# Performance work log

Measured on AMD Instinct MI355X. Metric: run time of the kernel, lower is better.

The kernel has to match this reference:

```python
import jax, jax.numpy as jnp
import numpy as np

INPUT_SIZE = 512
HIDDEN = 1024
OUT = 512
LN_EPS = 1e-5


def setup_inputs() -> dict:
    key = jax.random.key(0)
    ks = jax.random.split(key, 12)
    B, T = 128, 512
    def lin(k, fan_in, shape):
        bound = 1.0 / np.sqrt(fan_in)
        return jax.random.uniform(k, shape, jnp.float32, -bound, bound)
    in0 = INPUT_SIZE + HIDDEN
    in1 = HIDDEN + HIDDEN
    return {
        "x": jax.random.normal(ks[0], (B, T, INPUT_SIZE), jnp.float32),
        "W0": lin(ks[1], in0, (in0, 4 * HIDDEN)),
        "b0": lin(ks[2], in0, (4 * HIDDEN,)),
        "g0": jnp.ones((4 * HIDDEN,), jnp.float32),
        "beta0": jnp.zeros((4 * HIDDEN,), jnp.float32),
        "W1": lin(ks[3], in1, (in1, 4 * HIDDEN)),
        "b1": lin(ks[4], in1, (4 * HIDDEN,)),
        "g1": jnp.ones((4 * HIDDEN,), jnp.float32),
        "beta1": jnp.zeros((4 * HIDDEN,), jnp.float32),
        "fcW": lin(ks[5], HIDDEN, (HIDDEN, OUT)),
        "fcb": lin(ks[6], HIDDEN, (OUT,)),
    }


def _layer_norm(z, g, b):
    m = jnp.mean(z, axis=-1, keepdims=True)
    v = jnp.mean((z - m) ** 2, axis=-1, keepdims=True)
    return (z - m) * jax.lax.rsqrt(v + LN_EPS) * g + b


def _cell(xin, h, c, W, b, g, beta):
    comb = jnp.concatenate([xin, h], axis=-1)          # [B, in+H]
    gates = _layer_norm(comb @ W + b, g, beta)          # [B, 4H]
    i, f, gg, o = jnp.split(gates, 4, axis=-1)
    i, f, o = jax.nn.sigmoid(i), jax.nn.sigmoid(f), jax.nn.sigmoid(o)
    gg = jnp.tanh(gg)
    c_new = f * c + i * gg
    h_new = o * jnp.tanh(c_new)
    return h_new, c_new


def reference(x, W0, b0, g0, beta0, W1, b1, g1, beta1, fcW, fcb):
    B = x.shape[0]
    params = [(W0, b0, g0, beta0), (W1, b1, g1, beta1)]
    h0 = tuple(jnp.zeros((B, HIDDEN), x.dtype) for _ in range(2))
    c0 = tuple(jnp.zeros((B, HIDDEN), x.dtype) for _ in range(2))

    def step(carry, xt):
        hs, cs = carry
        inp = xt
        new_h, new_c = [], []
        for l, (W, b, g, beta) in enumerate(params):
            hl, cl = _cell(inp, hs[l], cs[l], W, b, g, beta)
            new_h.append(hl)
            new_c.append(cl)
            inp = hl
        return (tuple(new_h), tuple(new_c)), None

    xt = jnp.swapaxes(x, 0, 1)  # [T, B, D]
    (hs, _), _ = jax.lax.scan(step, (h0, c0), xt)
    return hs[-1] @ fcW + fcb  # [B, OUT]
```

## Files before the change

### kernel.cpp

```cpp
#include <hip/hip_runtime.h>
#include <hip/hip_bf16.h>

typedef __attribute__((ext_vector_type(8))) _Float16 half8_t;
typedef __attribute__((ext_vector_type(4))) float f32x4_t;
typedef unsigned long long u64;

#define SH 2056
#define HMOFF (16 * SH)
#define LDS_BYTES (2 * 16 * SH * 2)

__device__ __forceinline__ float sigm(float z) { return 1.0f / (1.0f + __expf(-z)); }
__device__ __forceinline__ float tanh_fast(float z) {
  float e = __expf(2.0f * z);
  return 1.0f - 2.0f / (e + 1.0f);
}

__device__ __forceinline__ half8_t ld_h8_coh(const _Float16* p) {
  union { half8_t h; u64 q[2]; } r;
  u64* q = (u64*)p;
  r.q[0] = __hip_atomic_load(q,     __ATOMIC_RELAXED, __HIP_MEMORY_SCOPE_SYSTEM);
  r.q[1] = __hip_atomic_load(q + 1, __ATOMIC_RELAXED, __HIP_MEMORY_SCOPE_SYSTEM);
  return r.h;
}
__device__ __forceinline__ void st_h_coh(_Float16* p, _Float16 v) {
  unsigned short b = __builtin_bit_cast(unsigned short, v);
  __hip_atomic_store((unsigned short*)p, b, __ATOMIC_RELAXED, __HIP_MEMORY_SCOPE_SYSTEM);
}
__device__ __forceinline__ float ld_f_coh(const float* p) {
  return __hip_atomic_load((float*)p, __ATOMIC_RELAXED, __HIP_MEMORY_SCOPE_SYSTEM);
}
__device__ __forceinline__ void st_f_coh(float* p, float v) {
  __hip_atomic_store(p, v, __ATOMIC_RELAXED, __HIP_MEMORY_SCOPE_SYSTEM);
}


__global__ void lstm_prep(const float* __restrict__ W0, const float* __restrict__ W1,
                          const float* __restrict__ b0, const float* __restrict__ g0,
                          const float* __restrict__ be0, const float* __restrict__ b1,
                          const float* __restrict__ g1, const float* __restrict__ be1,
                          _Float16* __restrict__ W0a, _Float16* __restrict__ W0b,
                          _Float16* __restrict__ W1a, _Float16* __restrict__ W1b,
                          float* __restrict__ vecs)
{
  int gid = blockIdx.x * 256 + threadIdx.x;
  const int W0N = 192 * 4096;
  const int W1N = 256 * 4096;
  if (gid < W0N) {
    int k8 = gid >> 12, gp = gid & 4095;
    int colgrp = gp >> 7, w = (gp >> 4) & 7, c = gp & 15;
    int gcol = ((c >> 2) << 10) + (colgrp << 5) + (w << 2) + (c & 3);
    half8_t va, vb;
    #pragma unroll
    for (int j = 0; j < 8; ++j) {
      float w32 = W0[(size_t)(k8 * 8 + j) * 4096 + gcol] * 32.0f;
      _Float16 p1 = (_Float16)w32;
      float r = w32 - (float)p1;
      va[j] = p1; vb[j] = (_Float16)(r * 2048.0f);
    }
    *(half8_t*)&W0a[(size_t)gp * 1536 + k8 * 8] = va;
    *(half8_t*)&W0b[(size_t)gp * 1536 + k8 * 8] = vb;
  } else if (gid < W0N + W1N) {
    int g2 = gid - W0N;
    int k8 = g2 >> 12, gp = g2 & 4095;
    int colgrp = gp >> 7, w = (gp >> 4) & 7, c = gp & 15;
    int gcol = ((c >> 2) << 10) + (colgrp << 5) + (w << 2) + (c & 3);
    half8_t va, vb;
    #pragma unroll
    for (int j = 0; j < 8; ++j) {
      float w32 = W1[(size_t)(k8 * 8 + j) * 4096 + gcol] * 32.0f;
      _Float16 p1 = (_Float16)w32;
      float r = w32 - (float)p1;
      va[j] = p1; vb[j] = (_Float16)(r * 2048.0f);
    }
    *(half8_t*)&W1a[(size_t)gp * 2048 + k8 * 8] = va;
    *(half8_t*)&W1b[(size_t)gp * 2048 + k8 * 8] = vb;
  } else if (gid < W0N + W1N + 6 * 4096) {
    int g2 = gid - W0N - W1N;
    int j = g2 >> 12, gp = g2 & 4095;
    int colgrp = gp >> 7, w = (gp >> 4) & 7, c = gp & 15;
    int gcol = ((c >> 2) << 10) + (colgrp << 5) + (w << 2) + (c & 3);
    const float* src = (j == 0) ? b0 : (j == 1) ? g0 : (j == 2) ? be0
                     : (j == 3) ? b1 : (j == 4) ? g1 : be1;
    vecs[j * 4096 + gp] = src[gcol];
  }
}

#define MFMA16(A, B, C) __builtin_amdgcn_mfma_f32_16x16x32_f16(A, B, C, 0, 0, 0)

__device__ __forceinline__ void groupbar(unsigned* bars, int grp, int tid, unsigned ep) {
  __syncthreads();
  if (tid == 0) {
    const int q = ep & 1;
    unsigned old = __hip_atomic_fetch_add(&bars[(grp * 2 + q) * 32], 1u,
                                          __ATOMIC_RELAXED, __HIP_MEMORY_SCOPE_AGENT);
    if (old == 31u) {
      __hip_atomic_store(&bars[(grp * 2 + q) * 32], 0u, __ATOMIC_RELAXED, __HIP_MEMORY_SCOPE_SYSTEM);
      __hip_atomic_store(&bars[1024 + grp * 32], ep, __ATOMIC_RELEASE, __HIP_MEMORY_SCOPE_SYSTEM);
    }
    while (__hip_atomic_load(&bars[1024 + grp * 32], __ATOMIC_RELAXED, __HIP_MEMORY_SCOPE_SYSTEM) < ep) {}
  }
  __syncthreads();
}

__global__ void __launch_bounds__(512, 2) lstm_seq(
    const float* __restrict__ x,
    const _Float16* __restrict__ W0ap,
    const _Float16* __restrict__ W0bp,
    const _Float16* __restrict__ W1ap,
    const _Float16* __restrict__ W1bp,
    const float* __restrict__ vecs,
    _Float16* __restrict__ hch,
    _Float16* __restrict__ hcm,
    float* __restrict__ stats,
    unsigned* __restrict__ bars,
    const float* __restrict__ fcW,
    const float* __restrict__ fcb,
    float* __restrict__ out)
{
  extern __shared__ _Float16 hS[];
  const int tid = threadIdx.x;
  const int wgid = blockIdx.x;
  const int mtile = wgid >> 5;
  const int colgrp = wgid & 31;
  const int wid = tid >> 6;
  const int lane = tid & 63;
  const int c16 = lane & 15;
  const int klo = lane >> 4;
  const int rowbase = mtile * 16;

  const int gp = colgrp * 128 + wid * 16 + c16;
  const float b0v  = vecs[gp];
  const float g0v  = vecs[4096 + gp];
  const float be0v = vecs[8192 + gp];
  const float b1v  = vecs[12288 + gp];
  const float g1v  = vecs[16384 + gp];
  const float be1v = vecs[20480 + gp];

  const int arow = rowbase + c16;
  const float* xbase = x + (size_t)arow * 512 * 512;
  const _Float16* w0a = W0ap + (size_t)gp * 1536;
  const _Float16* w0b = W0bp + (size_t)gp * 1536;
  const _Float16* w1a = W1ap + (size_t)gp * 2048;
  const _Float16* w1b = W1bp + (size_t)gp * 2048;
  const int repbase = (colgrp & 15) << 2;
  const int cbase = colgrp * 32 + wid * 4;

  float c0s[4] = {0,0,0,0};
  float c1s[4] = {0,0,0,0};
  unsigned ep = 0;
  half8_t stg[16];

#define STAGE_ISSUE() {                                                       \
    _Pragma("unroll")                                                         \
    for (int j = 0; j < 16; ++j) {                                            \
      int linear = tid + 512 * j;                                             \
      int plane = linear >> 12;                                               \
      int rem = linear & 4095;                                                \
      int row = rem >> 8;                                                     \
      int ck  = rem & 255;                                                    \
      const _Float16* srcp = (plane ? hcm : hch)                              \
                           + (size_t)(rowbase + row) * 2048 + ck * 8;         \
      stg[j] = ld_h8_coh(srcp);                                               \
    } }

#define STAGE_COMMIT() {                                                      \
    _Pragma("unroll")                                                         \
    for (int j = 0; j < 16; ++j) {                                            \
      int linear = tid + 512 * j;                                             \
      int plane = linear >> 12;                                               \
      int rem = linear & 4095;                                                \
      int row = rem >> 8;                                                     \
      int ck  = rem & 255;                                                    \
      *(half8_t*)&hS[plane * HMOFF + row * SH + ck * 8] = stg[j];             \
    }                                                                         \
    __syncthreads(); }

#define SPLIT2(E, J) { float e_ = (E); _Float16 h1_ = (_Float16)e_;           \
  float r_ = e_ - (float)h1_; ah[J] = h1_; am[J] = (_Float16)(r_ * 2048.0f); }

#define PROD3(HA, MA) \
  HA = MFMA16(ah, bh0, HA);                                                   \
  MA = MFMA16(ah, bm0, MA);                                                   \
  MA = MFMA16(am, bh0, MA);

#define X_BODY(KB, HA, MA) {                                                  \
      float4 xu = *(const float4*)(xp + (KB) * 32);                           \
      float4 xw = *(const float4*)(xp + (KB) * 32 + 4);                       \
      half8_t ah, am;                                                         \
      SPLIT2(xu.x, 0) SPLIT2(xu.y, 1) SPLIT2(xu.z, 2) SPLIT2(xu.w, 3)         \
      SPLIT2(xw.x, 4) SPLIT2(xw.y, 5) SPLIT2(xw.z, 6) SPLIT2(xw.w, 7)         \
      half8_t bh0 = *(const half8_t*)&w0a[(KB) * 32 + klo * 8];               \
      half8_t bm0 = *(const half8_t*)&w0b[(KB) * 32 + klo * 8];               \
      PROD3(HA, MA) }

#define H0_BODY(KB, HA, MA) {                                                 \
      half8_t ah = *(const half8_t*)&hS[c16 * SH + (KB) * 32 + klo * 8];      \
      half8_t am = *(const half8_t*)&hS[HMOFF + c16 * SH + (KB) * 32 + klo * 8]; \
      half8_t bh0 = *(const half8_t*)&w0a[512 + (KB) * 32 + klo * 8];         \
      half8_t bm0 = *(const half8_t*)&w0b[512 + (KB) * 32 + klo * 8];         \
      PROD3(HA, MA) }

#define H1_BODY(KB, HA, MA) {                                                 \
      half8_t ah = *(const half8_t*)&hS[c16 * SH + (KB) * 32 + klo * 8];      \
      half8_t am = *(const half8_t*)&hS[HMOFF + c16 * SH + (KB) * 32 + klo * 8]; \
      half8_t bh0 = *(const half8_t*)&w1a[(KB) * 32 + klo * 8];               \
      half8_t bm0 = *(const half8_t*)&w1b[(KB) * 32 + klo * 8];               \
      PROD3(HA, MA) }

#define STAT_ADD(V, BUF) {                                                    \
    _Pragma("unroll")                                                         \
    for (int r = 0; r < 4; ++r) {                                             \
      float s = V[r];                                                         \
      float q = V[r]*V[r];                                                    \
      _Pragma("unroll")                                                       \
      for (int m = 1; m <= 8; m <<= 1) { s += __shfl_xor(s, m); q += __shfl_xor(q, m); } \
      if (c16 == 0) {                                                         \
        int row = rowbase + klo * 4 + r;                                      \
        atomicAdd(&stats[(repbase + (BUF)) * 256 + row * 2 + 0], s);          \
        atomicAdd(&stats[(repbase + (BUF)) * 256 + row * 2 + 1], q);          \
      }                                                                       \
    } }

#define CELL(V, BUF, CS, GC, BEC, HB) {                                       \
    _Pragma("unroll")                                                         \
    for (int r = 0; r < 4; ++r) {                                             \
      int row = rowbase + klo * 4 + r;                                        \
      const float* sp = stats + ((c16 << 2) + (BUF)) * 256 + row * 2;         \
      float s_ = ld_f_coh(sp), q_ = ld_f_coh(sp + 1);                         \
      _Pragma("unroll")                                                       \
      for (int m = 1; m <= 8; m <<= 1) { s_ += __shfl_xor(s_, m); q_ += __shfl_xor(q_, m); } \
      float mean = s_ * (1.0f / 4096.0f);                                     \
      float msq  = q_ * (1.0f / 4096.0f);                                     \
      float rstd = rsqrtf(msq - mean * mean + 1e-5f);                         \
      float gh = (V[r] - mean) * rstd * GC + BEC;                             \
      float fg = __shfl_down(gh, 4);                                          \
      float gg = __shfl_down(gh, 8);                                          \
      float og = __shfl_down(gh, 12);                                         \
      if (c16 < 4) {                                                          \
        float iv = sigm(gh), fv = sigm(fg), zv = tanh_fast(gg), ov = sigm(og); \
        float cc = fv * CS[r] + iv * zv;                                      \
        CS[r] = cc;                                                           \
        float hv = ov * tanh_fast(cc);                                        \
        int idx = row * 2048 + (HB) + cbase + c16;                            \
        _Float16 h1v = (_Float16)hv;                                          \
        st_h_coh(&hch[idx], h1v);                                             \
        st_h_coh(&hcm[idx], (_Float16)((hv - (float)h1v) * 2048.0f));         \
      }                                                                       \
    } }

  f32x4_t ahe, aho, ame, amo;
  f32x4_t dhe, dho, dme, dmo;
  f32x4_t a0, d0;

#define A0_X(TT) {                                                            \
    ahe = {0,0,0,0}; aho = {0,0,0,0}; ame = {0,0,0,0}; amo = {0,0,0,0};       \
    const float* xp = xbase + (size_t)(TT) * 512 + klo * 8;                   \
    _Pragma("unroll 2")                                                       \
    for (int kb = 0; kb < 16; kb += 2) {                                      \
      X_BODY(kb,     ahe, ame);                                               \
      X_BODY(kb + 1, aho, amo);                                               \
    } }

#define A0_COMBINE() {                                                        \
    a0 = (ahe + aho) * 0.03125f + (ame + amo) * (1.0f / 65536.0f);            \
    _Pragma("unroll")                                                         \
    for (int r_ = 0; r_ < 4; ++r_) a0[r_] += b0v; }

  STAGE_ISSUE();
  STAGE_COMMIT();
  A0_X(0);
  #pragma unroll 2
  for (int kb = 0; kb < 32; kb += 2) {
    H0_BODY(kb,     ahe, ame);
    H0_BODY(kb + 1, aho, amo);
  }
  A0_COMBINE();
  STAT_ADD(a0, 0);
  groupbar(bars, mtile, tid, ++ep);
  CELL(a0, 0, c0s, g0v, be0v, 0);
  groupbar(bars, mtile, tid, ++ep);

  for (int t = 0; t < 512; ++t) {
    const int par = t & 1;
    const int npar = 1 - par;

    STAGE_ISSUE();
    if (t < 511) {
      A0_X(t + 1);
    }
    STAGE_COMMIT();

    dhe = {0,0,0,0}; dho = {0,0,0,0}; dme = {0,0,0,0}; dmo = {0,0,0,0};
    if (t < 511) {
      #pragma unroll 2
      for (int i = 0; i < 32; i += 2) {
        H1_BODY(2*i,     dhe, dme);
        H1_BODY(2*i+1,   dho, dmo);
        H0_BODY(i,       ahe, ame);
        H1_BODY(2*i+2,   dhe, dme);
        H1_BODY(2*i+3,   dho, dmo);
        H0_BODY(i+1,     aho, amo);
      }
    } else {
      #pragma unroll 2
      for (int kb = 0; kb < 64; kb += 2) {
        H1_BODY(kb,     dhe, dme);
        H1_BODY(kb + 1, dho, dmo);
      }
    }
    d0 = (dhe + dho) * 0.03125f + (dme + dmo) * (1.0f / 65536.0f);
    #pragma unroll
    for (int r = 0; r < 4; ++r) d0[r] += b1v;
    STAT_ADD(d0, 2 + par);

    if (t < 511) {
      A0_COMBINE();
      STAT_ADD(a0, npar);
    }

    if (colgrp < 16 && tid < 64) {
      int bufsel = ((tid >> 5) == 0) ? (2 + npar) : par;
      st_f_coh(&stats[((colgrp << 2) + bufsel) * 256 + mtile * 32 + (tid & 31)], 0.0f);
    }

    groupbar(bars, mtile, tid, ++ep);

    CELL(d0, 2 + par, c1s, g1v, be1v, 1024);
    if (t < 511) {
      CELL(a0, npar, c0s, g0v, be0v, 0);
    }
    groupbar(bars, mtile, tid, ++ep);
  }

  {
    if (tid < 256) {
      int b = rowbase + (tid >> 4);
      int o = colgrp * 16 + (tid & 15);
      const _Float16* p1 = hch + (size_t)b * 2048 + 1024;
      const _Float16* p2 = hcm + (size_t)b * 2048 + 1024;
      float s = fcb[o];
      #pragma unroll 4
      for (int k = 0; k < 1024; k += 4) {
        union { u64 q; _Float16 h[4]; } ua, um;
        ua.q = __hip_atomic_load((u64*)(p1 + k), __ATOMIC_RELAXED, __HIP_MEMORY_SCOPE_SYSTEM);
        um.q = __hip_atomic_load((u64*)(p2 + k), __ATOMIC_RELAXED, __HIP_MEMORY_SCOPE_SYSTEM);
        #pragma unroll
        for (int i = 0; i < 4; ++i) {
          float h = (float)ua.h[i] + (float)um.h[i] * (1.0f / 2048.0f);
          s = fmaf(h, fcW[(k + i) * 512 + o], s);
        }
      }
      out[b * 512 + o] = s;
    }
  }
}

extern "C" void kernel_launch(void* const* d_in, const int* in_sizes, int n_in,
                              void* d_out, int out_size, void* d_ws, size_t ws_size,
                              hipStream_t stream) {
  const float* x   = (const float*)d_in[0];
  const float* W0  = (const float*)d_in[1];
  const float* b0  = (const float*)d_in[2];
  const float* g0  = (const float*)d_in[3];
  const float* be0 = (const float*)d_in[4];
  const float* W1  = (const float*)d_in[5];
  const float* b1  = (const float*)d_in[6];
  const float* g1  = (const float*)d_in[7];
  const float* be1 = (const float*)d_in[8];
  const float* fcW = (const float*)d_in[9];
  const float* fcb = (const float*)d_in[10];
  float* out = (float*)d_out;

  char* ws = (char*)d_ws;
  _Float16* W0a  = (_Float16*)(ws);
  _Float16* W0b  = (_Float16*)(ws + 12582912);
  _Float16* W1a  = (_Float16*)(ws + 25165824);
  _Float16* W1b  = (_Float16*)(ws + 41943040);
  float* vecs    = (float*)(ws + 58720256);
  _Float16* hch  = (_Float16*)(ws + 58818560);
  _Float16* hcm  = (_Float16*)(ws + 59342848);
  float* stats   = (float*)(ws + 59867136);
  unsigned* bars = (unsigned*)(ws + 59932672);

  hipMemsetAsync(hch, 0, 524288 + 524288 + 65536 + 8192, stream);
  lstm_prep<<<7264, 256, 0, stream>>>(W0, W1, b0, g0, be0, b1, g1, be1,
                                      W0a, W0b, W1a, W1b, vecs);

  hipFuncSetAttribute((const void*)lstm_seq,
                      hipFuncAttributeMaxDynamicSharedMemorySize, LDS_BYTES);
  void* args[] = { (void*)&x, (void*)&W0a, (void*)&W0b, (void*)&W1a, (void*)&W1b,
                   (void*)&vecs, (void*)&hch, (void*)&hcm,
                   (void*)&stats, (void*)&bars,
                   (void*)&fcW, (void*)&fcb, (void*)&out };
  hipError_t lerr = hipLaunchCooperativeKernel((const void*)lstm_seq,
                                               dim3(256), dim3(512),
                                               args, LDS_BYTES, stream);
  if (lerr != hipSuccess) {
    (void)hipGetLastError();
    lstm_seq<<<dim3(256), dim3(512), LDS_BYTES, stream>>>(
        x, W0a, W0b, W1a, W1b, vecs, hch, hcm, stats, bars, fcW, fcb, out);
  }
}
```

Baseline: 36.77 ms.

## Remap workgroups by XCC so hidden-state exchange stays in local L2

At startup each workgroup reads its XCC id from a hardware register and claims a slot, so that all 32 workgroups sharing an m-tile sit on the same XCC. A new grid-wide barrier checks that the mapping is valid. When it is, the recurrent h exchange uses plain stores and sc0 L2-coherent loads instead of system-scope atomics, which targets cross-die coherence latency on every timestep. The fast path relies on the hardware scheduler placing exactly 32 workgroups per XCC and falls back to the old path otherwise. It also gives up overlapping the staging loads with the x projection.

Measured after the change: 44.78 ms. +21.8%, slower.

```diff
diff --git a/kernel.cpp b/kernel.cpp
--- a/kernel.cpp
+++ b/kernel.cpp
@@ -31,6 +31,13 @@
 }
 __device__ __forceinline__ void st_f_coh(float* p, float v) {
   __hip_atomic_store(p, v, __ATOMIC_RELAXED, __HIP_MEMORY_SCOPE_SYSTEM);
+}
+
+__device__ __forceinline__ half8_t ld_h8_l2(const _Float16* p) {
+  half8_t r;
+  asm volatile("global_load_dwordx4 %0, %1, off sc0"
+               : "=v"(r) : "v"(p) : "memory");
+  return r;
 }
 
 
@@ -87,6 +94,28 @@
 
 #define MFMA16(A, B, C) __builtin_amdgcn_mfma_f32_16x16x32_f16(A, B, C, 0, 0, 0)
 
+__device__ __forceinline__ void gridbar256(unsigned* bars, int wgid, int tid, unsigned ep) {
+  __syncthreads();
+  if (tid == 0) {
+    const int q = ep & 1;
+    unsigned old = __hip_atomic_fetch_add(&bars[(q * 8 + (wgid & 7)) * 32], 1u,
+                                          __ATOMIC_RELAXED, __HIP_MEMORY_SCOPE_AGENT);
+    if (old == 31u) {
+      unsigned mo = __hip_atomic_fetch_add(&bars[512 + q * 32], 1u,
+                                           __ATOMIC_RELAXED, __HIP_MEMORY_SCOPE_AGENT);
+      if (mo == 7u) {
+        #pragma unroll
+        for (int g = 0; g < 8; ++g)
+          __hip_atomic_store(&bars[(q * 8 + g) * 32], 0u, __ATOMIC_RELAXED, __HIP_MEMORY_SCOPE_SYSTEM);
+        __hip_atomic_store(&bars[512 + q * 32], 0u, __ATOMIC_RELAXED, __HIP_MEMORY_SCOPE_SYSTEM);
+        __hip_atomic_store(&bars[576], ep, __ATOMIC_RELEASE, __HIP_MEMORY_SCOPE_SYSTEM);
+      }
+    }
+    while (__hip_atomic_load(&bars[576], __ATOMIC_RELAXED, __HIP_MEMORY_SCOPE_SYSTEM) < ep) {}
+  }
+  __syncthreads();
+}
+
 __device__ __forceinline__ void groupbar(unsigned* bars, int grp, int tid, unsigned ep) {
   __syncthreads();
   if (tid == 0) {
@@ -118,14 +147,28 @@
     float* __restrict__ out)
 {
   extern __shared__ _Float16 hS[];
+  __shared__ unsigned sMeta[2];
   const int tid = threadIdx.x;
   const int wgid = blockIdx.x;
-  const int mtile = wgid >> 5;
-  const int colgrp = wgid & 31;
   const int wid = tid >> 6;
   const int lane = tid & 63;
   const int c16 = lane & 15;
   const int klo = lane >> 4;
+
+  if (tid == 0) {
+    unsigned xcc = __builtin_amdgcn_s_getreg((3 << 11) | 20) & 15u;
+    unsigned slot = __hip_atomic_fetch_add(&bars[1536 + (xcc & 7u)], 1u,
+                                           __ATOMIC_RELAXED, __HIP_MEMORY_SCOPE_AGENT);
+    if (slot >= 32u || xcc > 7u)
+      __hip_atomic_fetch_or(&bars[1544], 1u, __ATOMIC_ACQ_REL, __HIP_MEMORY_SCOPE_SYSTEM);
+    sMeta[0] = slot; sMeta[1] = xcc & 7u;
+  }
+  unsigned ep = 1;
+  gridbar256(bars, wgid, tid, ep);
+  const unsigned bad = __hip_atomic_load(&bars[1544], __ATOMIC_ACQUIRE, __HIP_MEMORY_SCOPE_SYSTEM);
+  const bool fast = (bad == 0u);
+  const int mtile  = fast ? (int)sMeta[1] : (wgid >> 5);
+  const int colgrp = fast ? (int)sMeta[0] : (wgid & 31);
   const int rowbase = mtile * 16;
 
   const int gp = colgrp * 128 + wid * 16 + c16;
@@ -147,10 +190,22 @@
 
   float c0s[4] = {0,0,0,0};
   float c1s[4] = {0,0,0,0};
-  unsigned ep = 0;
   half8_t stg[16];
 
-#define STAGE_ISSUE() {                                                       \
+#define STAGE_ADDR(J, SRCP)                                                   \
+      int linear = tid + 512 * (J);                                           \
+      int plane = linear >> 12;                                               \
+      int rem = linear & 4095;                                                \
+      int row = rem >> 8;                                                     \
+      int ck  = rem & 255;                                                    \
+      const _Float16* SRCP = (plane ? hcm : hch)                              \
+                           + (size_t)(rowbase + row) * 2048 + ck * 8;
+
+#define STAGE_FAST() {                                                        \
+    _Pragma("unroll")                                                         \
+    for (int j = 0; j < 16; ++j) { STAGE_ADDR(j, srcp) stg[j] = ld_h8_l2(srcp); } \
+    asm volatile("s_waitcnt vmcnt(0)" ::: "memory");                          \
+    __builtin_amdgcn_sched_barrier(0);                                        \
     _Pragma("unroll")                                                         \
     for (int j = 0; j < 16; ++j) {                                            \
       int linear = tid + 512 * j;                                             \
@@ -158,10 +213,13 @@
       int rem = linear & 4095;                                                \
       int row = rem >> 8;                                                     \
       int ck  = rem & 255;                                                    \
-      const _Float16* srcp = (plane ? hcm : hch)                              \
-                           + (size_t)(rowbase + row) * 2048 + ck * 8;         \
-      stg[j] = ld_h8_coh(srcp);                                               \
-    } }
+      *(half8_t*)&hS[plane * HMOFF + row * SH + ck * 8] = stg[j];             \
+    }                                                                         \
+    __syncthreads(); }
+
+#define STAGE_ISSUE() {                                                       \
+    _Pragma("unroll")                                                         \
+    for (int j = 0; j < 16; ++j) { STAGE_ADDR(j, srcp) stg[j] = ld_h8_coh(srcp); } }
 
 #define STAGE_COMMIT() {                                                      \
     _Pragma("unroll")                                                         \
@@ -243,8 +301,9 @@
         float hv = ov * tanh_fast(cc);                                        \
         int idx = row * 2048 + (HB) + cbase + c16;                            \
         _Float16 h1v = (_Float16)hv;                                          \
-        st_h_coh(&hch[idx], h1v);                                             \
-        st_h_coh(&hcm[idx], (_Float16)((hv - (float)h1v) * 2048.0f));         \
+        _Float16 h2v = (_Float16)((hv - (float)h1v) * 2048.0f);               \
+        if (fast) { hch[idx] = h1v; hcm[idx] = h2v; }                         \
+        else { st_h_coh(&hch[idx], h1v); st_h_coh(&hcm[idx], h2v); }          \
       }                                                                       \
     } }
 
@@ -266,8 +325,8 @@
     _Pragma("unroll")                                                         \
     for (int r_ = 0; r_ < 4; ++r_) a0[r_] += b0v; }
 
-  STAGE_ISSUE();
-  STAGE_COMMIT();
+  if (fast) { STAGE_FAST(); }
+  else { STAGE_ISSUE(); STAGE_COMMIT(); }
   A0_X(0);
   #pragma unroll 2
   for (int kb = 0; kb < 32; kb += 2) {
@@ -284,11 +343,14 @@
     const int par = t & 1;
     const int npar = 1 - par;
 
-    STAGE_ISSUE();
-    if (t < 511) {
-      A0_X(t + 1);
-    }
-    STAGE_COMMIT();
+    if (fast) {
+      STAGE_FAST();
+      if (t < 511) A0_X(t + 1);
+    } else {
+      STAGE_ISSUE();
+      if (t < 511) A0_X(t + 1);
+      STAGE_COMMIT();
+    }
 
     dhe = {0,0,0,0}; dho = {0,0,0,0}; dme = {0,0,0,0}; dmo = {0,0,0,0};
     if (t < 511) {
```

## Split LDS staging of hidden state into halves and overlap second commit with compute

Applied to the files above, without the earlier changes.

The staged hidden-state copy into LDS is split into two halves (first and second 1024 columns). Only the first half is committed before the fused layer-0/layer-1 MFMA loop starts, and the second half is committed midway, before the remaining layer-1 K blocks. The aim is to shorten the critical path before compute can begin and overlap part of the LDS write with MFMA work. The cost is an extra __syncthreads per timestep and a reordered loop interleaving, which may reduce ILP.

Measured after the change: 36.26 ms. Within noise of the previous version (-1.4%).

```diff
diff --git a/kernel.cpp b/kernel.cpp
--- a/kernel.cpp
+++ b/kernel.cpp
@@ -150,28 +150,42 @@
   unsigned ep = 0;
   half8_t stg[16];
 
-#define STAGE_ISSUE() {                                                       \
-    _Pragma("unroll")                                                         \
-    for (int j = 0; j < 16; ++j) {                                            \
-      int linear = tid + 512 * j;                                             \
-      int plane = linear >> 12;                                               \
-      int rem = linear & 4095;                                                \
-      int row = rem >> 8;                                                     \
-      int ck  = rem & 255;                                                    \
+#define HDECODE(Q)                                                            \
+      int idx = tid + 512 * (Q);                                              \
+      int plane = idx >> 11;                                                  \
+      int rem = idx & 2047;                                                   \
+      int row = rem >> 7;                                                     \
+      int ckk = rem & 127;
+
+#define STAGE_ISSUE_ALL() {                                                   \
+    _Pragma("unroll")                                                         \
+    for (int q = 0; q < 8; ++q) {                                             \
+      HDECODE(q)                                                              \
       const _Float16* srcp = (plane ? hcm : hch)                              \
-                           + (size_t)(rowbase + row) * 2048 + ck * 8;         \
-      stg[j] = ld_h8_coh(srcp);                                               \
+                           + (size_t)(rowbase + row) * 2048 + ckk * 8;        \
+      stg[q] = ld_h8_coh(srcp);                                               \
+    }                                                                         \
+    _Pragma("unroll")                                                         \
+    for (int q = 0; q < 8; ++q) {                                             \
+      HDECODE(q)                                                              \
+      const _Float16* srcp = (plane ? hcm : hch)                              \
+                           + (size_t)(rowbase + row) * 2048 + 1024 + ckk * 8; \
+      stg[8 + q] = ld_h8_coh(srcp);                                           \
     } }
 
-#define STAGE_COMMIT() {                                                      \
-    _Pragma("unroll")                                                         \
-    for (int j = 0; j < 16; ++j) {                                            \
-      int linear = tid + 512 * j;                                             \
-      int plane = linear >> 12;                                               \
-      int rem = linear & 4095;                                                \
-      int row = rem >> 8;                                                     \
-      int ck  = rem & 255;                                                    \
-      *(half8_t*)&hS[plane * HMOFF + row * SH + ck * 8] = stg[j];             \
+#define STAGE_COMMIT_H0() {                                                   \
+    _Pragma("unroll")                                                         \
+    for (int q = 0; q < 8; ++q) {                                             \
+      HDECODE(q)                                                              \
+      *(half8_t*)&hS[plane * HMOFF + row * SH + ckk * 8] = stg[q];            \
+    }                                                                         \
+    __syncthreads(); }
+
+#define STAGE_COMMIT_H1() {                                                   \
+    _Pragma("unroll")                                                         \
+    for (int q = 0; q < 8; ++q) {                                             \
+      HDECODE(q)                                                              \
+      *(half8_t*)&hS[plane * HMOFF + row * SH + 1024 + ckk * 8] = stg[8 + q]; \
     }                                                                         \
     __syncthreads(); }
 
@@ -266,8 +280,9 @@
     _Pragma("unroll")                                                         \
     for (int r_ = 0; r_ < 4; ++r_) a0[r_] += b0v; }
 
-  STAGE_ISSUE();
-  STAGE_COMMIT();
+  STAGE_ISSUE_ALL();
+  STAGE_COMMIT_H0();
+  STAGE_COMMIT_H1();
   A0_X(0);
   #pragma unroll 2
   for (int kb = 0; kb < 32; kb += 2) {
@@ -284,26 +299,36 @@
     const int par = t & 1;
     const int npar = 1 - par;
 
-    STAGE_ISSUE();
+    STAGE_ISSUE_ALL();
     if (t < 511) {
       A0_X(t + 1);
     }
-    STAGE_COMMIT();
+    STAGE_COMMIT_H0();
 
     dhe = {0,0,0,0}; dho = {0,0,0,0}; dme = {0,0,0,0}; dmo = {0,0,0,0};
     if (t < 511) {
       #pragma unroll 2
       for (int i = 0; i < 32; i += 2) {
-        H1_BODY(2*i,     dhe, dme);
-        H1_BODY(2*i+1,   dho, dmo);
+        H1_BODY(i,       dhe, dme);
+        H1_BODY(i + 1,   dho, dmo);
         H0_BODY(i,       ahe, ame);
-        H1_BODY(2*i+2,   dhe, dme);
-        H1_BODY(2*i+3,   dho, dmo);
-        H0_BODY(i+1,     aho, amo);
+        H0_BODY(i + 1,   aho, amo);
+      }
+      STAGE_COMMIT_H1();
+      #pragma unroll 2
+      for (int kb = 32; kb < 64; kb += 2) {
+        H1_BODY(kb,     dhe, dme);
+        H1_BODY(kb + 1, dho, dmo);
       }
     } else {
       #pragma unroll 2
-      for (int kb = 0; kb < 64; kb += 2) {
+      for (int kb = 0; kb < 32; kb += 2) {
+        H1_BODY(kb,     dhe, dme);
+        H1_BODY(kb + 1, dho, dmo);
+      }
+      STAGE_COMMIT_H1();
+      #pragma unroll 2
+      for (int kb = 32; kb < 64; kb += 2) {
         H1_BODY(kb,     dhe, dme);
         H1_BODY(kb + 1, dho, dmo);
       }
```
